# Optimization experiments

Measured on AMD Instinct MI355X. Metric: run time of the kernel, lower is better.

The kernel has to match this reference:

```python
import jax, jax.numpy as jnp
import numpy as np

K = 7          # kernel_size from init
PAD = (K - 1) // 2
EPS = 1e-8


def _local_std(x):
    """Per-pixel std of the zero-padded KxK x C neighborhood, matching
    torch: unfold(pad=3) -> mean over dim=1 (C*K*K) -> sqrt(mean(d^2)+eps).
    Computed with box-filter convolutions instead of materializing the
    49x-blown-up unfold tensor.
    Returns [B, H*W].
    """
    B, C, H, W = x.shape
    n = C * K * K  # fixed divisor (zero padding counts toward the mean)
    ones = jnp.ones((1, C, K, K), x.dtype)  # OIHW: sums over channels + window
    s = jax.lax.conv_general_dilated(x, ones, (1, 1), [(PAD, PAD), (PAD, PAD)])      # [B,1,H,W]
    s2 = jax.lax.conv_general_dilated(x * x, ones, (1, 1), [(PAD, PAD), (PAD, PAD)])  # [B,1,H,W]
    mu = s / n
    var = s2 / n - mu * mu  # E[x^2] - mu^2 == mean((x-mu)^2)
    return jnp.sqrt(var + EPS).reshape(B, H * W)


def _smooth_l1_mean(a, b):
    d = a - b
    ad = jnp.abs(d)
    per = jnp.where(ad < 1.0, 0.5 * d * d, ad - 0.5)
    return jnp.mean(per)


def setup_inputs() -> dict:
    key = jax.random.key(0)
    k1, k2 = jax.random.split(key)
    shape = (16, 3, 512, 512)
    pred_moire = jax.random.normal(k1, shape, dtype=jnp.float32)
    moire = jax.random.normal(k2, shape, dtype=jnp.float32)
    return {"pred_moire": pred_moire, "moire": moire}


def reference(pred_moire, moire):
    std_pred = _local_std(pred_moire)  # [B, H*W]
    std_tgt = _local_std(moire)        # [B, H*W]
    return _smooth_l1_mean(std_pred, std_tgt)  # scalar
```

## Files before the change

### kernel.cpp

```cpp
#include <hip/hip_runtime.h>


#define K     7
#define PAD   3
#define TSX   64
#define TSY   32
#define HR    (TSY + K - 1)
#define LDSW  68
#define NT    256

__device__ __forceinline__ float4 add3(float4 a, float4 b, float4 c) {
    return make_float4(a.x + b.x + c.x, a.y + b.y + c.y,
                       a.z + b.z + c.z, a.w + b.w + c.w);
}
__device__ __forceinline__ float4 sq3(float4 a, float4 b, float4 c) {
    return make_float4(fmaf(a.x, a.x, fmaf(b.x, b.x, c.x * c.x)),
                       fmaf(a.y, a.y, fmaf(b.y, b.y, c.y * c.y)),
                       fmaf(a.z, a.z, fmaf(b.z, b.z, c.z * c.z)),
                       fmaf(a.w, a.w, fmaf(b.w, b.w, c.w * c.w)));
}

__global__ __launch_bounds__(NT, 4) void dist_loss_kernel(
    const float* __restrict__ pred,
    const float* __restrict__ tgt,
    float* __restrict__ out)
{
    constexpr int   C = 3, H = 512, W = 512;
    constexpr float INV_N     = 1.0f / (C * K * K);
    constexpr float INV_TOTAL = 1.0f / (16.0f * 512.0f * 512.0f);

    __shared__ float sh_s[HR][LDSW];
    __shared__ float sh_q[HR][LDSW];

    const int    tid  = threadIdx.x;
    const int    tx0  = blockIdx.x * TSX;
    const int    ty0  = blockIdx.y * TSY;
    const int    b    = blockIdx.z;
    const size_t plane = (size_t)H * W;
    const float4 z4 = make_float4(0.f, 0.f, 0.f, 0.f);

    float4 pA, pB;
    float  acc = 0.0f;

    #pragma unroll
    for (int which = 0; which < 2; ++which) {
        const float* base = (which == 0 ? pred : tgt) + (size_t)b * C * plane;

        for (int task = tid; task < HR * 16; task += NT) {
            const int   row = task >> 4;
            const int   cg  = task & 15;
            const int   gy  = ty0 - PAD + row;
            const float m   = ((unsigned)gy < (unsigned)H) ? 1.0f : 0.0f;
            const int   gyc = min(max(gy, 0), H - 1);
            const int   gx0 = tx0 + (cg << 2);
            const bool  leftOK  = (gx0 > 0);
            const bool  rightOK = (gx0 < 508);

            const float* r0 = base + (size_t)gyc * W + gx0;
            const float* r1 = r0 + plane;
            const float* r2 = r1 + plane;

            float4 A0 = leftOK  ? *(const float4*)(r0 - 4) : z4;
            float4 B0 = *(const float4*)(r0);
            float4 C0 = rightOK ? *(const float4*)(r0 + 4) : z4;
            float4 A1 = leftOK  ? *(const float4*)(r1 - 4) : z4;
            float4 B1 = *(const float4*)(r1);
            float4 C1 = rightOK ? *(const float4*)(r1 + 4) : z4;
            float4 A2 = leftOK  ? *(const float4*)(r2 - 4) : z4;
            float4 B2 = *(const float4*)(r2);
            float4 C2 = rightOK ? *(const float4*)(r2 + 4) : z4;

            float4 tl = add3(A0, A1, A2);
            float4 tm = add3(B0, B1, B2);
            float4 tr = add3(C0, C1, C2);
            float4 ul = sq3(A0, A1, A2);
            float4 um = sq3(B0, B1, B2);
            float4 ur = sq3(C0, C1, C2);

            float h0 = tl.y + tl.z + tl.w + tm.x + tm.y + tm.z + tm.w;
            float h1 = h0 - tl.y + tr.x;
            float h2 = h1 - tl.z + tr.y;
            float h3 = h2 - tl.w + tr.z;
            float g0 = ul.y + ul.z + ul.w + um.x + um.y + um.z + um.w;
            float g1 = g0 - ul.y + ur.x;
            float g2 = g1 - ul.z + ur.y;
            float g3 = g2 - ul.w + ur.z;

            *(float4*)&sh_s[row][cg << 2] =
                make_float4(h0 * m, h1 * m, h2 * m, h3 * m);
            *(float4*)&sh_q[row][cg << 2] =
                make_float4(g0 * m, g1 * m, g2 * m, g3 * m);
        }
        __syncthreads();

        {
            const int rp = tid >> 4;
            const int x  = (tid & 15) << 2;

            float4 S = z4, Q = z4;
            #pragma unroll
            for (int k = 0; k < K; ++k) {
                float4 hv = *(const float4*)&sh_s[2 * rp + k][x];
                float4 gv = *(const float4*)&sh_q[2 * rp + k][x];
                S.x += hv.x; S.y += hv.y; S.z += hv.z; S.w += hv.w;
                Q.x += gv.x; Q.y += gv.y; Q.z += gv.z; Q.w += gv.w;
            }
            float4 hA = *(const float4*)&sh_s[2 * rp][x];
            float4 gA = *(const float4*)&sh_q[2 * rp][x];
            float4 hB = *(const float4*)&sh_s[2 * rp + 7][x];
            float4 gB = *(const float4*)&sh_q[2 * rp + 7][x];
            float4 S2 = make_float4(S.x - hA.x + hB.x, S.y - hA.y + hB.y,
                                    S.z - hA.z + hB.z, S.w - hA.w + hB.w);
            float4 Q2 = make_float4(Q.x - gA.x + gB.x, Q.y - gA.y + gB.y,
                                    Q.z - gA.z + gB.z, Q.w - gA.w + gB.w);

            #define STD4(Sv, Qv, D)                                           \
                {                                                             \
                    float mux = (Sv).x * INV_N, muy = (Sv).y * INV_N,         \
                          muz = (Sv).z * INV_N, muw = (Sv).w * INV_N;         \
                    (D).x = sqrtf(fmaf(-mux, mux, (Qv).x * INV_N) + 1e-8f);   \
                    (D).y = sqrtf(fmaf(-muy, muy, (Qv).y * INV_N) + 1e-8f);   \
                    (D).z = sqrtf(fmaf(-muz, muz, (Qv).z * INV_N) + 1e-8f);   \
                    (D).w = sqrtf(fmaf(-muw, muw, (Qv).w * INV_N) + 1e-8f);   \
                }
            #define SL1(a, bb)                                                \
                {                                                             \
                    float d  = (a) - (bb);                                    \
                    float ad = fabsf(d);                                      \
                    acc += (ad < 1.0f) ? 0.5f * d * d : (ad - 0.5f);          \
                }

            if (which == 0) {
                STD4(S, Q, pA);
                STD4(S2, Q2, pB);
            } else {
                float4 sA, sB;
                STD4(S, Q, sA);
                STD4(S2, Q2, sB);
                SL1(pA.x, sA.x); SL1(pA.y, sA.y);
                SL1(pA.z, sA.z); SL1(pA.w, sA.w);
                SL1(pB.x, sB.x); SL1(pB.y, sB.y);
                SL1(pB.z, sB.z); SL1(pB.w, sB.w);
            }
            #undef STD4
            #undef SL1
        }
        __syncthreads();
    }

    #pragma unroll
    for (int off = 32; off > 0; off >>= 1)
        acc += __shfl_down(acc, off, 64);

    __shared__ float wave_sums[NT / 64];
    if ((tid & 63) == 0) wave_sums[tid >> 6] = acc;
    __syncthreads();
    if (tid == 0) {
        float s = 0.0f;
        #pragma unroll
        for (int w = 0; w < NT / 64; ++w) s += wave_sums[w];
        atomicAdd(out, s * INV_TOTAL);
    }
}

extern "C" void kernel_launch(void* const* d_in, const int* in_sizes, int n_in,
                              void* d_out, int out_size, void* d_ws, size_t ws_size,
                              hipStream_t stream) {
    const float* pred = (const float*)d_in[0];
    const float* tgt  = (const float*)d_in[1];
    float* out = (float*)d_out;

    hipMemsetAsync(out, 0, sizeof(float), stream);

    dim3 grid(512 / TSX, 512 / TSY, 16);
    dist_loss_kernel<<<grid, NT, 0, stream>>>(pred, tgt, out);
}
```

Before: 144.9 us.

## Rewrite as single-wave column-streaming kernel with sliding vertical window

Replaces the 256-thread two-pass tile kernel with a 64-thread single-wave block in which each lane owns one column and streams down 16 output rows. Horizontal box sums go through a small LDS strip with no barriers, relying only on wave-level lgkmcnt waits. Vertical sums use a register ring buffer as a sliding window, and pred and target are processed together in the same pass. Global loads are scalar per-lane rather than float4 and the row halo is reloaded per 16-row strip, which raises redundant traffic. Correctness depends on the whole block being a single wavefront.

```diff
diff --git a/kernel.cpp b/kernel.cpp
--- a/kernel.cpp
+++ b/kernel.cpp
@@ -1,166 +1,131 @@
 #include <hip/hip_runtime.h>
 
 
-#define K     7
-#define PAD   3
-#define TSX   64
-#define TSY   32
-#define HR    (TSY + K - 1)
-#define LDSW  68
-#define NT    256
-
-__device__ __forceinline__ float4 add3(float4 a, float4 b, float4 c) {
-    return make_float4(a.x + b.x + c.x, a.y + b.y + c.y,
-                       a.z + b.z + c.z, a.w + b.w + c.w);
-}
-__device__ __forceinline__ float4 sq3(float4 a, float4 b, float4 c) {
-    return make_float4(fmaf(a.x, a.x, fmaf(b.x, b.x, c.x * c.x)),
-                       fmaf(a.y, a.y, fmaf(b.y, b.y, c.y * c.y)),
-                       fmaf(a.z, a.z, fmaf(b.z, b.z, c.z * c.z)),
-                       fmaf(a.w, a.w, fmaf(b.w, b.w, c.w * c.w)));
-}
+#define SH    16
+#define NR    (SH + 6)
+#define NT    64
+#define STR   5
 
 __global__ __launch_bounds__(NT, 4) void dist_loss_kernel(
     const float* __restrict__ pred,
     const float* __restrict__ tgt,
     float* __restrict__ out)
 {
-    constexpr int   C = 3, H = 512, W = 512;
-    constexpr float INV_N     = 1.0f / (C * K * K);
+    constexpr int   W = 512, H = 512;
+    constexpr float INV_N     = 1.0f / 147.0f;
     constexpr float INV_TOTAL = 1.0f / (16.0f * 512.0f * 512.0f);
 
-    __shared__ float sh_s[HR][LDSW];
-    __shared__ float sh_q[HR][LDSW];
+    __shared__ float sh[72 * STR];
 
-    const int    tid  = threadIdx.x;
-    const int    tx0  = blockIdx.x * TSX;
-    const int    ty0  = blockIdx.y * TSY;
-    const int    b    = blockIdx.z;
+    const int l  = threadIdx.x;
+    const int x0 = blockIdx.x * 64;
+    const int ys = blockIdx.y * SH;
+    const int b  = blockIdx.z;
+
     const size_t plane = (size_t)H * W;
-    const float4 z4 = make_float4(0.f, 0.f, 0.f, 0.f);
+    const float* bp = pred + (size_t)b * 3 * plane;
+    const float* bt = tgt  + (size_t)b * 3 * plane;
 
-    float4 pA, pB;
-    float  acc = 0.0f;
+    const int   colM   = x0 + l - 4;
+    const int   cMain  = max(colM, 0);
+    const int   colH   = x0 + 60 + min(l, 7);
+    const int   cHalo  = min(colH, W - 1);
+    const float mMainC = (colM >= 0) ? 1.f : 0.f;
+    const float mHaloC = (colH < W) ? 1.f : 0.f;
+    const bool  haloLn = (l < 8);
 
+    float rh0[8], rg0[8], rh1[8], rg1[8];
     #pragma unroll
-    for (int which = 0; which < 2; ++which) {
-        const float* base = (which == 0 ? pred : tgt) + (size_t)b * C * plane;
+    for (int r = 0; r < 8; ++r) { rh0[r] = rg0[r] = rh1[r] = rg1[r] = 0.f; }
+    float S0 = 0.f, Q0 = 0.f, S1 = 0.f, Q1 = 0.f, acc = 0.f;
 
-        for (int task = tid; task < HR * 16; task += NT) {
-            const int   row = task >> 4;
-            const int   cg  = task & 15;
-            const int   gy  = ty0 - PAD + row;
-            const float m   = ((unsigned)gy < (unsigned)H) ? 1.0f : 0.0f;
-            const int   gyc = min(max(gy, 0), H - 1);
-            const int   gx0 = tx0 + (cg << 2);
-            const bool  leftOK  = (gx0 > 0);
-            const bool  rightOK = (gx0 < 508);
+    float A0[2], A1[2], A2[2], B0[2], B1[2], B2[2];
+    float h0v[2], h1v[2], h2v[2], h3v[2], h4v[2], h5v[2];
 
-            const float* r0 = base + (size_t)gyc * W + gx0;
-            const float* r1 = r0 + plane;
-            const float* r2 = r1 + plane;
+    #define LOADROW(P, r_) do {                                              \
+        const int gyc_ = min(max(ys - 3 + (r_), 0), H - 1);                  \
+        const float* rp_ = bp + (size_t)gyc_ * W;                            \
+        const float* rt_ = bt + (size_t)gyc_ * W;                            \
+        A0[P] = rp_[cMain];  A1[P] = rp_[plane + cMain];                     \
+        A2[P] = rp_[2 * plane + cMain];                                      \
+        B0[P] = rt_[cMain];  B1[P] = rt_[plane + cMain];                     \
+        B2[P] = rt_[2 * plane + cMain];                                      \
+        h0v[P] = rp_[cHalo]; h1v[P] = rp_[plane + cHalo];                    \
+        h2v[P] = rp_[2 * plane + cHalo];                                     \
+        h3v[P] = rt_[cHalo]; h4v[P] = rt_[plane + cHalo];                    \
+        h5v[P] = rt_[2 * plane + cHalo];                                     \
+    } while (0)
 
-            float4 A0 = leftOK  ? *(const float4*)(r0 - 4) : z4;
-            float4 B0 = *(const float4*)(r0);
-            float4 C0 = rightOK ? *(const float4*)(r0 + 4) : z4;
-            float4 A1 = leftOK  ? *(const float4*)(r1 - 4) : z4;
-            float4 B1 = *(const float4*)(r1);
-            float4 C1 = rightOK ? *(const float4*)(r1 + 4) : z4;
-            float4 A2 = leftOK  ? *(const float4*)(r2 - 4) : z4;
-            float4 B2 = *(const float4*)(r2);
-            float4 C2 = rightOK ? *(const float4*)(r2 + 4) : z4;
+    #define FENCE() asm volatile("s_waitcnt lgkmcnt(0)" ::: "memory")
 
-            float4 tl = add3(A0, A1, A2);
-            float4 tm = add3(B0, B1, B2);
-            float4 tr = add3(C0, C1, C2);
-            float4 ul = sq3(A0, A1, A2);
-            float4 um = sq3(B0, B1, B2);
-            float4 ur = sq3(C0, C1, C2);
+    #define CONSUME(i_, P, JN, JO) do {                                      \
+        const int   gy_ = ys - 3 + (i_);                                     \
+        const float rm_ = ((unsigned)gy_ < (unsigned)H) ? 1.f : 0.f;         \
+        const float mM_ = mMainC * rm_;                                      \
+        const float mH_ = mHaloC * rm_;                                      \
+        float t0 = (A0[P] + A1[P] + A2[P]) * mM_;                            \
+        float u0 = fmaf(A0[P], A0[P],                                        \
+                   fmaf(A1[P], A1[P], A2[P] * A2[P])) * mM_;                 \
+        float t1 = (B0[P] + B1[P] + B2[P]) * mM_;                            \
+        float u1 = fmaf(B0[P], B0[P],                                        \
+                   fmaf(B1[P], B1[P], B2[P] * B2[P])) * mM_;                 \
+        float th0 = (h0v[P] + h1v[P] + h2v[P]) * mH_;                        \
+        float uh0 = fmaf(h0v[P], h0v[P],                                     \
+                    fmaf(h1v[P], h1v[P], h2v[P] * h2v[P])) * mH_;            \
+        float th1 = (h3v[P] + h4v[P] + h5v[P]) * mH_;                        \
+        float uh1 = fmaf(h3v[P], h3v[P],                                     \
+                    fmaf(h4v[P], h4v[P], h5v[P] * h5v[P])) * mH_;            \
+        FENCE();        \
+        sh[l * STR + 0] = t0;  sh[l * STR + 1] = u0;                         \
+        sh[l * STR + 2] = t1;  sh[l * STR + 3] = u1;                         \
+        if (haloLn) {                                                        \
+            sh[(64 + l) * STR + 0] = th0; sh[(64 + l) * STR + 1] = uh0;      \
+            sh[(64 + l) * STR + 2] = th1; sh[(64 + l) * STR + 3] = uh1;      \
+        }                                                                    \
+        FENCE();   \
+        float hh0 = 0.f, gg0 = 0.f, hh1 = 0.f, gg1 = 0.f;                    \
+        _Pragma("unroll")                                                    \
+        for (int j2 = 1; j2 <= 7; ++j2) {                                    \
+            const float* q_ = &sh[(l + j2) * STR];                           \
+            hh0 += q_[0]; gg0 += q_[1]; hh1 += q_[2]; gg1 += q_[3];          \
+        }                                                                    \
+        S0 += hh0 - rh0[JO]; rh0[JN] = hh0;                                  \
+        Q0 += gg0 - rg0[JO]; rg0[JN] = gg0;                                  \
+        S1 += hh1 - rh1[JO]; rh1[JN] = hh1;                                  \
+        Q1 += gg1 - rg1[JO]; rg1[JN] = gg1;                                  \
+        if ((i_) >= 6) {                                                     \
+            float mu0 = S0 * INV_N;                                          \
+            float sd0 = sqrtf(fmaf(-mu0, mu0, Q0 * INV_N) + 1e-8f);          \
+            float mu1 = S1 * INV_N;                                          \
+            float sd1 = sqrtf(fmaf(-mu1, mu1, Q1 * INV_N) + 1e-8f);          \
+            float d_  = sd0 - sd1;                                           \
+            float ad_ = fabsf(d_);                                           \
+            acc += (ad_ < 1.f) ? 0.5f * d_ * d_ : (ad_ - 0.5f);              \
+        }                                                                    \
+    } while (0)
 
-            float h0 = tl.y + tl.z + tl.w + tm.x + tm.y + tm.z + tm.w;
-            float h1 = h0 - tl.y + tr.x;
-            float h2 = h1 - tl.z + tr.y;
-            float h3 = h2 - tl.w + tr.z;
-            float g0 = ul.y + ul.z + ul.w + um.x + um.y + um.z + um.w;
-            float g1 = g0 - ul.y + ur.x;
-            float g2 = g1 - ul.z + ur.y;
-            float g3 = g2 - ul.w + ur.z;
+    LOADROW(0, 0);
 
-            *(float4*)&sh_s[row][cg << 2] =
-                make_float4(h0 * m, h1 * m, h2 * m, h3 * m);
-            *(float4*)&sh_q[row][cg << 2] =
-                make_float4(g0 * m, g1 * m, g2 * m, g3 * m);
+    #pragma unroll 1
+    for (int g = 0; g < 3; ++g) {
+        #pragma unroll
+        for (int j = 0; j < 8; ++j) {
+            const int i = g * 8 + j;
+            if (i < NR) {
+                LOADROW((j + 1) & 1, i + 1);
+                CONSUME(i, j & 1, j, (j + 1) & 7);
+            }
         }
-        __syncthreads();
+    }
 
-        {
-            const int rp = tid >> 4;
-            const int x  = (tid & 15) << 2;
-
-            float4 S = z4, Q = z4;
-            #pragma unroll
-            for (int k = 0; k < K; ++k) {
-                float4 hv = *(const float4*)&sh_s[2 * rp + k][x];
-                float4 gv = *(const float4*)&sh_q[2 * rp + k][x];
-                S.x += hv.x; S.y += hv.y; S.z += hv.z; S.w += hv.w;
-                Q.x += gv.x; Q.y += gv.y; Q.z += gv.z; Q.w += gv.w;
-            }
-            float4 hA = *(const float4*)&sh_s[2 * rp][x];
-            float4 gA = *(const float4*)&sh_q[2 * rp][x];
-            float4 hB = *(const float4*)&sh_s[2 * rp + 7][x];
-            float4 gB = *(const float4*)&sh_q[2 * rp + 7][x];
-            float4 S2 = make_float4(S.x - hA.x + hB.x, S.y - hA.y + hB.y,
-                                    S.z - hA.z + hB.z, S.w - hA.w + hB.w);
-            float4 Q2 = make_float4(Q.x - gA.x + gB.x, Q.y - gA.y + gB.y,
-                                    Q.z - gA.z + gB.z, Q.w - gA.w + gB.w);
-
-            #define STD4(Sv, Qv, D)                                           \
-                {                                                             \
-                    float mux = (Sv).x * INV_N, muy = (Sv).y * INV_N,         \
-                          muz = (Sv).z * INV_N, muw = (Sv).w * INV_N;         \
-                    (D).x = sqrtf(fmaf(-mux, mux, (Qv).x * INV_N) + 1e-8f);   \
-                    (D).y = sqrtf(fmaf(-muy, muy, (Qv).y * INV_N) + 1e-8f);   \
-                    (D).z = sqrtf(fmaf(-muz, muz, (Qv).z * INV_N) + 1e-8f);   \
-                    (D).w = sqrtf(fmaf(-muw, muw, (Qv).w * INV_N) + 1e-8f);   \
-                }
-            #define SL1(a, bb)                                                \
-                {                                                             \
-                    float d  = (a) - (bb);                                    \
-                    float ad = fabsf(d);                                      \
-                    acc += (ad < 1.0f) ? 0.5f * d * d : (ad - 0.5f);          \
-                }
-
-            if (which == 0) {
-                STD4(S, Q, pA);
-                STD4(S2, Q2, pB);
-            } else {
-                float4 sA, sB;
-                STD4(S, Q, sA);
-                STD4(S2, Q2, sB);
-                SL1(pA.x, sA.x); SL1(pA.y, sA.y);
-                SL1(pA.z, sA.z); SL1(pA.w, sA.w);
-                SL1(pB.x, sB.x); SL1(pB.y, sB.y);
-                SL1(pB.z, sB.z); SL1(pB.w, sB.w);
-            }
-            #undef STD4
-            #undef SL1
-        }
-        __syncthreads();
-    }
+    #undef CONSUME
+    #undef FENCE
+    #undef LOADROW
 
     #pragma unroll
     for (int off = 32; off > 0; off >>= 1)
         acc += __shfl_down(acc, off, 64);
-
-    __shared__ float wave_sums[NT / 64];
-    if ((tid & 63) == 0) wave_sums[tid >> 6] = acc;
-    __syncthreads();
-    if (tid == 0) {
-        float s = 0.0f;
-        #pragma unroll
-        for (int w = 0; w < NT / 64; ++w) s += wave_sums[w];
-        atomicAdd(out, s * INV_TOTAL);
-    }
+    if (l == 0) atomicAdd(out, acc * INV_TOTAL);
 }
 
 extern "C" void kernel_launch(void* const* d_in, const int* in_sizes, int n_in,
@@ -172,6 +137,6 @@
 
     hipMemsetAsync(out, 0, sizeof(float), stream);
 
-    dim3 grid(512 / TSX, 512 / TSY, 16);
+    dim3 grid(512 / 64, 512 / SH, 16);
     dist_loss_kernel<<<grid, NT, 0, stream>>>(pred, tgt, out);
 }
```

New measurement: 170.8 us. 17.9% more time.
